# Kernel optimization log

Measured on AMD Instinct MI355X. Metric: run time of the kernel, lower is better.

Reference implementation:

```python
import jax, jax.numpy as jnp
import numpy as np

K_NEIGHBORS = 8   # num_neighbors init arg
BETA = 0.5        # smooth-L1 beta
EPS = 1e-8        # torch cosine_similarity eps


def setup_inputs() -> dict:
    key = jax.random.key(0)
    k1, k2, k3 = jax.random.split(key, 3)
    B, N, D, C = 16, 1024, 768, 2
    return {
        "student_emb": jax.random.normal(k1, (B, N, D), dtype=jnp.float32),
        "teacher_emb": jax.random.normal(k2, (B, N, D), dtype=jnp.float32),
        "centers": jax.random.normal(k3, (B, N, C), dtype=jnp.float32),
    }


def _cosine(anchor, nb):
    # anchor [B,N,1,D], nb [B,N,K,D] -> [B,N,K]
    dot = jnp.sum(anchor * nb, axis=-1)
    na = jnp.maximum(jnp.linalg.norm(anchor, axis=-1), EPS)
    nb_n = jnp.maximum(jnp.linalg.norm(nb, axis=-1), EPS)
    return dot / (na * nb_n)


def reference(student_emb, teacher_emb, centers):
    B, N, _ = centers.shape
    k = min(K_NEIGHBORS + 1, N)
    # brute-force pairwise squared distances [B,N,N] (knn_points)
    sq = jnp.sum(centers * centers, axis=-1)
    d2 = sq[:, :, None] + sq[:, None, :] - 2.0 * jnp.einsum("bnc,bmc->bnm", centers, centers)
    _, idx = jax.lax.top_k(-d2, k)   # ascending distance; idx [B,N,k]
    idx = idx[:, :, 1:]               # drop self (distance 0 is first)
    # knn_gather: neighbors [B,N,K,D]
    gather = jax.vmap(lambda e, i: e[i])
    student_nb = gather(student_emb, idx)
    teacher_nb = gather(teacher_emb, idx)
    student_rel = _cosine(student_emb[:, :, None, :], student_nb)  # [B,N,K]
    teacher_rel = jax.lax.stop_gradient(_cosine(teacher_emb[:, :, None, :], teacher_nb))
    diff = jnp.abs(student_rel - teacher_rel)
    sl1 = jnp.where(diff < BETA, 0.5 * diff * diff / BETA, diff - 0.5 * BETA)
    per_patch = sl1.mean(axis=-1)  # [B,N]
    return per_patch.mean()        # reduction='mean'
```

## Files before the change

kernel.cpp:

```cpp
#include <hip/hip_runtime.h>
#include <hip/hip_fp16.h>
#include <math.h>

#define BB 16
#define NN 1024
#define DD 768
#define KK 8
#define BETA_F 0.5f
#define EPS_F 1e-8f

#define TPK_BLOCKS ((BB * NN) / 8)
#define NORM_BLOCKS ((BB * NN) / 4)

typedef _Float16 h2_t __attribute__((ext_vector_type(2)));

#if defined(__has_builtin)
#if __has_builtin(__builtin_amdgcn_fdot2)
#define HAVE_FDOT2 1
#endif
#endif

__device__ __forceinline__ float dot4acc(uint2 a, uint2 b, float acc) {
#ifdef HAVE_FDOT2
    acc = __builtin_amdgcn_fdot2(__builtin_bit_cast(h2_t, a.x),
                                 __builtin_bit_cast(h2_t, b.x), acc, false);
    acc = __builtin_amdgcn_fdot2(__builtin_bit_cast(h2_t, a.y),
                                 __builtin_bit_cast(h2_t, b.y), acc, false);
#else
    float2 fa = __half22float2(__builtin_bit_cast(__half2, a.x));
    float2 fb = __half22float2(__builtin_bit_cast(__half2, b.x));
    acc = fmaf(fa.x, fb.x, acc); acc = fmaf(fa.y, fb.y, acc);
    fa = __half22float2(__builtin_bit_cast(__half2, a.y));
    fb = __half22float2(__builtin_bit_cast(__half2, b.y));
    acc = fmaf(fa.x, fb.x, acc); acc = fmaf(fa.y, fb.y, acc);
#endif
    return acc;
}

__device__ __forceinline__ unsigned wave_min_u32_to_all(unsigned x) {
    int v = (int)x;
#define STEP(CTRL, RM) {                                                    \
        int y_ = __builtin_amdgcn_update_dpp(v, v, CTRL, RM, 0xf, false);   \
        v = (int)((unsigned)v < (unsigned)y_ ? (unsigned)v : (unsigned)y_); \
    }
    STEP(0x111, 0xf)
    STEP(0x112, 0xf)
    STEP(0x114, 0xf)
    STEP(0x118, 0xf)
    STEP(0x142, 0xa)
    STEP(0x143, 0xc)
#undef STEP
    return (unsigned)__builtin_amdgcn_readlane(v, 63);
}

__device__ __forceinline__ unsigned topk_u(float anx, float any_, float sqn, float4 c) {
    float dot = anx * c.x + any_ * c.y;
    float d2  = (sqn + c.z) - 2.0f * dot;
    unsigned int u = __float_as_uint(d2);
    u ^= (unsigned int)((int)u >> 31) | 0x80000000u;
    return u;
}

struct KeysU { unsigned k[16]; };

#define PIN_KEYSU(K)                                                        \
    asm("" : "+v"(K.k[0]),  "+v"(K.k[1]),  "+v"(K.k[2]),  "+v"(K.k[3]),    \
             "+v"(K.k[4]),  "+v"(K.k[5]),  "+v"(K.k[6]),  "+v"(K.k[7]),    \
             "+v"(K.k[8]),  "+v"(K.k[9]),  "+v"(K.k[10]), "+v"(K.k[11]),   \
             "+v"(K.k[12]), "+v"(K.k[13]), "+v"(K.k[14]), "+v"(K.k[15]))

__device__ __forceinline__ void initkeysu(KeysU& K, float anx, float any_, float sqn,
                                          const float4* c4, int lane) {
#pragma unroll
    for (int i = 0; i < 16; ++i) {
        const int m_ = i * 64 + lane;
        K.k[i] = topk_u(anx, any_, sqn, c4[m_]);
    }
}

__device__ __forceinline__ unsigned umin2(unsigned a, unsigned b) { return a < b ? a : b; }

__device__ __forceinline__ unsigned mintreeu(const KeysU& K) {
    return umin2(umin2(umin2(umin2(K.k[0], K.k[1]),  umin2(K.k[2], K.k[3])),
                       umin2(umin2(K.k[4], K.k[5]),  umin2(K.k[6], K.k[7]))),
                 umin2(umin2(umin2(K.k[8], K.k[9]),  umin2(K.k[10], K.k[11])),
                       umin2(umin2(K.k[12], K.k[13]), umin2(K.k[14], K.k[15]))));
}

__device__ __forceinline__ void topk_wave_body(const float* __restrict__ centers,
                                               int* __restrict__ idx_out,
                                               int tb, int tid, float4* c4) {
    const int b    = tb >> 7;
    const int grp  = tb & 127;
    const int wave = tid >> 6;
    const int lane = tid & 63;

    const float4* cbase = (const float4*)(centers + (size_t)b * NN * 2);
    for (int i = tid; i < NN / 2; i += 256) {
        float4 v = cbase[i];
        c4[2 * i + 0] = make_float4(v.x, v.y, v.x * v.x + v.y * v.y, 0.f);
        c4[2 * i + 1] = make_float4(v.z, v.w, v.z * v.z + v.w * v.w, 0.f);
    }
    __syncthreads();

    const int nA = grp * 8 + wave * 2;
    const int nB = nA + 1;
    const float4 cA = c4[nA];
    const float4 cB = c4[nB];

    KeysU KA, KB;
    initkeysu(KA, cA.x, cA.y, cA.z, c4, lane);
    initkeysu(KB, cB.x, cB.y, cB.z, c4, lane);
    PIN_KEYSU(KA);
    PIN_KEYSU(KB);

    unsigned lmA = mintreeu(KA);
    unsigned lmB = mintreeu(KB);
    int mmA[9], mmB[9];

#pragma unroll
    for (int r = 0; r < 9; ++r) {
        const unsigned gA = wave_min_u32_to_all(lmA);
        const unsigned gB = wave_min_u32_to_all(lmB);

        unsigned mA = 0xffffffffu, mB = 0xffffffffu;
#pragma unroll
        for (int i = 15; i >= 0; --i) {
            unsigned long long bA = __ballot(KA.k[i] == gA);
            unsigned long long bB = __ballot(KB.k[i] == gB);
            mA = bA ? (unsigned)(i * 64) + (unsigned)__builtin_ctzll(bA) : mA;
            mB = bB ? (unsigned)(i * 64) + (unsigned)__builtin_ctzll(bB) : mB;
        }
        mmA[r] = (int)mA;
        mmB[r] = (int)mB;

        const unsigned iwA = mA >> 6, lwA = mA & 63;
        const unsigned iwB = mB >> 6, lwB = mB & 63;
        const bool winA = ((unsigned)lane == lwA);
        const bool winB = ((unsigned)lane == lwB);
#pragma unroll
        for (int i = 0; i < 16; ++i) {
            KA.k[i] = ((unsigned)i == iwA && winA) ? 0xffffffffu : KA.k[i];
            KB.k[i] = ((unsigned)i == iwB && winB) ? 0xffffffffu : KB.k[i];
        }
        PIN_KEYSU(KA);
        PIN_KEYSU(KB);
        lmA = mintreeu(KA);
        lmB = mintreeu(KB);
    }

    if (lane == 0) {
        int* outp = idx_out + ((size_t)b * NN + nA) * KK;
        ((int4*)outp)[0] = make_int4(mmA[1], mmA[2], mmA[3], mmA[4]);
        ((int4*)outp)[1] = make_int4(mmA[5], mmA[6], mmA[7], mmA[8]);
        ((int4*)outp)[2] = make_int4(mmB[1], mmB[2], mmB[3], mmB[4]);
        ((int4*)outp)[3] = make_int4(mmB[5], mmB[6], mmB[7], mmB[8]);
    }
}

__device__ __forceinline__ void normh_body(const float* __restrict__ s,
                                           const float* __restrict__ t,
                                           __half* __restrict__ ns,
                                           __half* __restrict__ nt,
                                           int nb, int tid) {
    const int row  = nb * 4 + (tid >> 6);
    const int lane = tid & 63;
    const float4* srow = (const float4*)(s + (size_t)row * DD);
    const float4* trow = (const float4*)(t + (size_t)row * DD);
    float4 vs[3], vt[3];
    float ss = 0.f, tt = 0.f;
#pragma unroll
    for (int i = 0; i < 3; ++i) {
        vs[i] = srow[lane + 64 * i];
        vt[i] = trow[lane + 64 * i];
        ss = fmaf(vs[i].x, vs[i].x, fmaf(vs[i].y, vs[i].y,
             fmaf(vs[i].z, vs[i].z, fmaf(vs[i].w, vs[i].w, ss))));
        tt = fmaf(vt[i].x, vt[i].x, fmaf(vt[i].y, vt[i].y,
             fmaf(vt[i].z, vt[i].z, fmaf(vt[i].w, vt[i].w, tt))));
    }
#pragma unroll
    for (int m = 1; m < 64; m <<= 1) {
        ss += __shfl_xor(ss, m);
        tt += __shfl_xor(tt, m);
    }
    const float is_ = 1.0f / fmaxf(sqrtf(ss), EPS_F);
    const float it_ = 1.0f / fmaxf(sqrtf(tt), EPS_F);

    uint2* nsrow = (uint2*)(ns + (size_t)row * DD);
    uint2* ntrow = (uint2*)(nt + (size_t)row * DD);
#pragma unroll
    for (int i = 0; i < 3; ++i) {
        __half2 a0 = __floats2half2_rn(vs[i].x * is_, vs[i].y * is_);
        __half2 a1 = __floats2half2_rn(vs[i].z * is_, vs[i].w * is_);
        __half2 b0 = __floats2half2_rn(vt[i].x * it_, vt[i].y * it_);
        __half2 b1 = __floats2half2_rn(vt[i].z * it_, vt[i].w * it_);
        uint2 ua; ua.x = __builtin_bit_cast(unsigned int, a0);
        ua.y = __builtin_bit_cast(unsigned int, a1);
        uint2 ub; ub.x = __builtin_bit_cast(unsigned int, b0);
        ub.y = __builtin_bit_cast(unsigned int, b1);
        nsrow[lane + 64 * i] = ua;
        ntrow[lane + 64 * i] = ub;
    }
}

__global__ __launch_bounds__(256) void fused_prep(const float* __restrict__ centers,
                                                  const float* __restrict__ s,
                                                  const float* __restrict__ t,
                                                  int* __restrict__ idx_out,
                                                  __half* __restrict__ ns,
                                                  __half* __restrict__ nt) {
    __shared__ float4 c4[NN];
    const int r3 = blockIdx.x % 3;
    const int q3 = blockIdx.x / 3;
    if (r3 == 0)
        topk_wave_body(centers, idx_out, q3, threadIdx.x, c4);
    else
        normh_body(s, t, ns, nt, q3 * 2 + (r3 - 1), threadIdx.x);
}

__global__ __launch_bounds__(256) void topk_kernel(const float* __restrict__ centers,
                                                   int* __restrict__ idx_out) {
    __shared__ float4 c4[NN];
    topk_wave_body(centers, idx_out, blockIdx.x, threadIdx.x, c4);
}

__global__ __launch_bounds__(256) void lossh_kernel(const __half* __restrict__ ns,
                                                    const __half* __restrict__ nt,
                                                    const int* __restrict__ idx,
                                                    float* __restrict__ part) {
    const int bid  = blockIdx.x;
    const int v    = (bid & 7) * 512 + (bid >> 3);
    const int wave = threadIdx.x >> 6;
    const int lane = threadIdx.x & 63;
    const int p    = v * 4 + wave;
    const int base = p & ~(NN - 1);

    int q[8];
    {
        const int4* ip = (const int4*)(idx + (size_t)p * KK);
        int4 a = ip[0], c = ip[1];
        q[0] = base + a.x; q[1] = base + a.y; q[2] = base + a.z; q[3] = base + a.w;
        q[4] = base + c.x; q[5] = base + c.y; q[6] = base + c.z; q[7] = base + c.w;
    }

    const uint2* srow = (const uint2*)(ns + (size_t)p * DD);
    const uint2* trow = (const uint2*)(nt + (size_t)p * DD);
    uint2 sa[3], ta[3];
#pragma unroll
    for (int c = 0; c < 3; ++c) {
        sa[c] = srow[lane + 64 * c];
        ta[c] = trow[lane + 64 * c];
    }

    uint2 sv[8][3], tv[8][3];
#pragma unroll
    for (int j = 0; j < 8; ++j) {
        const uint2* snb = (const uint2*)(ns + (size_t)q[j] * DD);
        const uint2* tnb = (const uint2*)(nt + (size_t)q[j] * DD);
#pragma unroll
        for (int c = 0; c < 3; ++c) {
            sv[j][c] = snb[lane + 64 * c];
            tv[j][c] = tnb[lane + 64 * c];
        }
    }

    float ds[8], dt[8];
#pragma unroll
    for (int j = 0; j < 8; ++j) {
        float a = 0.f, b = 0.f;
#pragma unroll
        for (int c = 0; c < 3; ++c) {
            a = dot4acc(sa[c], sv[j][c], a);
            b = dot4acc(ta[c], tv[j][c], b);
        }
        ds[j] = a;
        dt[j] = b;
    }
#pragma unroll
    for (int m = 1; m < 64; m <<= 1) {
#pragma unroll
        for (int j = 0; j < 8; ++j) {
            ds[j] += __shfl_xor(ds[j], m);
            dt[j] += __shfl_xor(dt[j], m);
        }
    }
    float sum = 0.f;
#pragma unroll
    for (int j = 0; j < 8; ++j) {
        const float diff = fabsf(ds[j] - dt[j]);
        sum += diff < BETA_F ? (0.5f * diff * diff / BETA_F) : (diff - 0.5f * BETA_F);
    }

    __shared__ float wpart[4];
    if (lane == 0) wpart[wave] = sum;
    __syncthreads();
    if (threadIdx.x == 0)
        part[v] = (wpart[0] + wpart[1]) + (wpart[2] + wpart[3]);
}

__global__ __launch_bounds__(256) void norm_kernel(const float* __restrict__ s,
                                                   const float* __restrict__ t,
                                                   float* __restrict__ inv_s,
                                                   float* __restrict__ inv_t) {
    const int row  = blockIdx.x * 4 + (threadIdx.x >> 6);
    const int lane = threadIdx.x & 63;
    const float4* srow = (const float4*)(s + (size_t)row * DD);
    const float4* trow = (const float4*)(t + (size_t)row * DD);
    float ss = 0.f, tt = 0.f;
#pragma unroll
    for (int i = 0; i < 3; ++i) {
        float4 v = srow[lane + 64 * i];
        ss = fmaf(v.x, v.x, fmaf(v.y, v.y, fmaf(v.z, v.z, fmaf(v.w, v.w, ss))));
        float4 w = trow[lane + 64 * i];
        tt = fmaf(w.x, w.x, fmaf(w.y, w.y, fmaf(w.z, w.z, fmaf(w.w, w.w, tt))));
    }
#pragma unroll
    for (int m = 1; m < 64; m <<= 1) {
        ss += __shfl_xor(ss, m);
        tt += __shfl_xor(tt, m);
    }
    if (lane == 0) {
        inv_s[row] = 1.0f / fmaxf(sqrtf(ss), EPS_F);
        inv_t[row] = 1.0f / fmaxf(sqrtf(tt), EPS_F);
    }
}

__global__ __launch_bounds__(256) void lossf_kernel(const float* __restrict__ s,
                                                    const float* __restrict__ t,
                                                    const int* __restrict__ idx,
                                                    const float* __restrict__ inv_s,
                                                    const float* __restrict__ inv_t,
                                                    float* __restrict__ part) {
    const int wave = threadIdx.x >> 6;
    const int lane = threadIdx.x & 63;
    const int p    = blockIdx.x * 4 + wave;
    const int base = p & ~(NN - 1);
    int q[8];
    {
        const int4* ip = (const int4*)(idx + (size_t)p * KK);
        int4 a = ip[0], c = ip[1];
        q[0] = base + a.x; q[1] = base + a.y; q[2] = base + a.z; q[3] = base + a.w;
        q[4] = base + c.x; q[5] = base + c.y; q[6] = base + c.z; q[7] = base + c.w;
    }
    float isq[8], itq[8];
#pragma unroll
    for (int j = 0; j < 8; ++j) { isq[j] = inv_s[q[j]]; itq[j] = inv_t[q[j]]; }
    const float isn = inv_s[p];
    const float itn = inv_t[p];
    const float4* srow = (const float4*)(s + (size_t)p * DD);
    const float4* trow = (const float4*)(t + (size_t)p * DD);
    float4 as0 = srow[lane], as1 = srow[lane + 64], as2 = srow[lane + 128];
    float4 at0 = trow[lane], at1 = trow[lane + 64], at2 = trow[lane + 128];
    float ds[8], dt[8];
#pragma unroll
    for (int j = 0; j < 8; ++j) {
        const float4* snb = (const float4*)(s + (size_t)q[j] * DD);
        const float4* tnb = (const float4*)(t + (size_t)q[j] * DD);
        float4 v0 = snb[lane], v1 = snb[lane + 64], v2 = snb[lane + 128];
        float4 w0 = tnb[lane], w1 = tnb[lane + 64], w2 = tnb[lane + 128];
        float a = 0.f, b = 0.f;
        a = fmaf(as0.x, v0.x, a); a = fmaf(as0.y, v0.y, a);
        a = fmaf(as0.z, v0.z, a); a = fmaf(as0.w, v0.w, a);
        a = fmaf(as1.x, v1.x, a); a = fmaf(as1.y, v1.y, a);
        a = fmaf(as1.z, v1.z, a); a = fmaf(as1.w, v1.w, a);
        a = fmaf(as2.x, v2.x, a); a = fmaf(as2.y, v2.y, a);
        a = fmaf(as2.z, v2.z, a); a = fmaf(as2.w, v2.w, a);
        b = fmaf(at0.x, w0.x, b); b = fmaf(at0.y, w0.y, b);
        b = fmaf(at0.z, w0.z, b); b = fmaf(at0.w, w0.w, b);
        b = fmaf(at1.x, w1.x, b); b = fmaf(at1.y, w1.y, b);
        b = fmaf(at1.z, w1.z, b); b = fmaf(at1.w, w1.w, b);
        b = fmaf(at2.x, w2.x, b); b = fmaf(at2.y, w2.y, b);
        b = fmaf(at2.z, w2.z, b); b = fmaf(at2.w, w2.w, b);
        ds[j] = a; dt[j] = b;
    }
#pragma unroll
    for (int m = 1; m < 64; m <<= 1) {
#pragma unroll
        for (int j = 0; j < 8; ++j) {
            ds[j] += __shfl_xor(ds[j], m);
            dt[j] += __shfl_xor(dt[j], m);
        }
    }
    float sum = 0.f;
#pragma unroll
    for (int j = 0; j < 8; ++j) {
        const float cs   = ds[j] * isn * isq[j];
        const float ct   = dt[j] * itn * itq[j];
        const float diff = fabsf(cs - ct);
        sum += diff < BETA_F ? (0.5f * diff * diff / BETA_F) : (diff - 0.5f * BETA_F);
    }
    __shared__ float wpart[4];
    if (lane == 0) wpart[wave] = sum;
    __syncthreads();
    if (threadIdx.x == 0)
        part[blockIdx.x] = (wpart[0] + wpart[1]) + (wpart[2] + wpart[3]);
}

__global__ __launch_bounds__(256) void finalize_kernel(const float* __restrict__ part,
                                                       float* __restrict__ out) {
    __shared__ float red[256];
    float acc = 0.f;
    for (int i = threadIdx.x; i < (BB * NN) / 4; i += 256) acc += part[i];
    red[threadIdx.x] = acc;
    __syncthreads();
    for (int off = 128; off > 0; off >>= 1) {
        if (threadIdx.x < off) red[threadIdx.x] += red[threadIdx.x + off];
        __syncthreads();
    }
    if (threadIdx.x == 0) out[0] = red[0] * (1.0f / (float)(BB * NN * KK));
}

extern "C" void kernel_launch(void* const* d_in, const int* in_sizes, int n_in,
                              void* d_out, int out_size, void* d_ws, size_t ws_size,
                              hipStream_t stream) {
    const float* student = (const float*)d_in[0];
    const float* teacher = (const float*)d_in[1];
    const float* centers = (const float*)d_in[2];
    float* out = (float*)d_out;

    const size_t idx_bytes  = (size_t)BB * NN * KK * sizeof(int);
    const size_t half_bytes = (size_t)BB * NN * DD * sizeof(__half);
    const size_t part_bytes = 4096 * sizeof(float);
    int* idx_buf = (int*)d_ws;

    if (ws_size >= idx_bytes + 2 * half_bytes + part_bytes) {
        __half* ns  = (__half*)((char*)d_ws + idx_bytes);
        __half* nt  = ns + (size_t)BB * NN * DD;
        float* part = (float*)((char*)d_ws + idx_bytes + 2 * half_bytes);
        fused_prep<<<TPK_BLOCKS + NORM_BLOCKS, 256, 0, stream>>>(centers, student,
                                                                 teacher, idx_buf, ns, nt);
        lossh_kernel<<<NORM_BLOCKS, 256, 0, stream>>>(ns, nt, idx_buf, part);
        finalize_kernel<<<1, 256, 0, stream>>>(part, out);
    } else {
        float* inv_s = (float*)((char*)d_ws + idx_bytes);
        float* inv_t = inv_s + BB * NN;
        float* part  = inv_t + BB * NN;
        topk_kernel<<<TPK_BLOCKS, 256, 0, stream>>>(centers, idx_buf);
        norm_kernel<<<NORM_BLOCKS, 256, 0, stream>>>(student, teacher, inv_s, inv_t);
        lossf_kernel<<<NORM_BLOCKS, 256, 0, stream>>>(student, teacher, idx_buf,
                                                      inv_s, inv_t, part);
        finalize_kernel<<<1, 256, 0, stream>>>(part, out);
    }
}
```

Measured before the change: 81.87 us.

## Split fused prep into separate top-k and normalize kernels, roll selection loop

Replaces the single fused_prep kernel, which interleaved top-k blocks and normalization blocks in one launch, with two separate launches: topk_kernel and normh_kernel. It also removes the inline-asm register pinning of the key arrays, stops unrolling the 9-round selection loop, and writes each neighbor index to global memory as soon as it is found instead of buffering them and storing int4 vectors at the end. This trades the overlap of compute-bound top-k with bandwidth-bound normalization for smaller code and possibly lower register pressure. It adds a kernel launch boundary and uses scalar stores.

```diff
diff --git a/kernel.cpp b/kernel.cpp
--- a/kernel.cpp
+++ b/kernel.cpp
@@ -63,12 +63,6 @@
 
 struct KeysU { unsigned k[16]; };
 
-#define PIN_KEYSU(K)                                                        \
-    asm("" : "+v"(K.k[0]),  "+v"(K.k[1]),  "+v"(K.k[2]),  "+v"(K.k[3]),    \
-             "+v"(K.k[4]),  "+v"(K.k[5]),  "+v"(K.k[6]),  "+v"(K.k[7]),    \
-             "+v"(K.k[8]),  "+v"(K.k[9]),  "+v"(K.k[10]), "+v"(K.k[11]),   \
-             "+v"(K.k[12]), "+v"(K.k[13]), "+v"(K.k[14]), "+v"(K.k[15]))
-
 __device__ __forceinline__ void initkeysu(KeysU& K, float anx, float any_, float sqn,
                                           const float4* c4, int lane) {
 #pragma unroll
@@ -111,14 +105,14 @@
     KeysU KA, KB;
     initkeysu(KA, cA.x, cA.y, cA.z, c4, lane);
     initkeysu(KB, cB.x, cB.y, cB.z, c4, lane);
-    PIN_KEYSU(KA);
-    PIN_KEYSU(KB);
 
     unsigned lmA = mintreeu(KA);
     unsigned lmB = mintreeu(KB);
-    int mmA[9], mmB[9];
-
-#pragma unroll
+
+    int* rowA = idx_out + ((size_t)b * NN + nA) * KK;
+    int* rowB = rowA + KK;
+
+#pragma unroll 1
     for (int r = 0; r < 9; ++r) {
         const unsigned gA = wave_min_u32_to_all(lmA);
         const unsigned gB = wave_min_u32_to_all(lmB);
@@ -131,8 +125,11 @@
             mA = bA ? (unsigned)(i * 64) + (unsigned)__builtin_ctzll(bA) : mA;
             mB = bB ? (unsigned)(i * 64) + (unsigned)__builtin_ctzll(bB) : mB;
         }
-        mmA[r] = (int)mA;
-        mmB[r] = (int)mB;
+
+        if (r > 0 && lane == 0) {
+            rowA[r - 1] = (int)mA;
+            rowB[r - 1] = (int)mB;
+        }
 
         const unsigned iwA = mA >> 6, lwA = mA & 63;
         const unsigned iwB = mB >> 6, lwB = mB & 63;
@@ -143,28 +140,23 @@
             KA.k[i] = ((unsigned)i == iwA && winA) ? 0xffffffffu : KA.k[i];
             KB.k[i] = ((unsigned)i == iwB && winB) ? 0xffffffffu : KB.k[i];
         }
-        PIN_KEYSU(KA);
-        PIN_KEYSU(KB);
         lmA = mintreeu(KA);
         lmB = mintreeu(KB);
     }
-
-    if (lane == 0) {
-        int* outp = idx_out + ((size_t)b * NN + nA) * KK;
-        ((int4*)outp)[0] = make_int4(mmA[1], mmA[2], mmA[3], mmA[4]);
-        ((int4*)outp)[1] = make_int4(mmA[5], mmA[6], mmA[7], mmA[8]);
-        ((int4*)outp)[2] = make_int4(mmB[1], mmB[2], mmB[3], mmB[4]);
-        ((int4*)outp)[3] = make_int4(mmB[5], mmB[6], mmB[7], mmB[8]);
-    }
-}
-
-__device__ __forceinline__ void normh_body(const float* __restrict__ s,
-                                           const float* __restrict__ t,
-                                           __half* __restrict__ ns,
-                                           __half* __restrict__ nt,
-                                           int nb, int tid) {
-    const int row  = nb * 4 + (tid >> 6);
-    const int lane = tid & 63;
+}
+
+__global__ __launch_bounds__(256) void topk_kernel(const float* __restrict__ centers,
+                                                   int* __restrict__ idx_out) {
+    __shared__ float4 c4[NN];
+    topk_wave_body(centers, idx_out, blockIdx.x, threadIdx.x, c4);
+}
+
+__global__ __launch_bounds__(256) void normh_kernel(const float* __restrict__ s,
+                                                    const float* __restrict__ t,
+                                                    __half* __restrict__ ns,
+                                                    __half* __restrict__ nt) {
+    const int row  = blockIdx.x * 4 + (threadIdx.x >> 6);
+    const int lane = threadIdx.x & 63;
     const float4* srow = (const float4*)(s + (size_t)row * DD);
     const float4* trow = (const float4*)(t + (size_t)row * DD);
     float4 vs[3], vt[3];
@@ -201,27 +193,6 @@
         nsrow[lane + 64 * i] = ua;
         ntrow[lane + 64 * i] = ub;
     }
-}
-
-__global__ __launch_bounds__(256) void fused_prep(const float* __restrict__ centers,
-                                                  const float* __restrict__ s,
-                                                  const float* __restrict__ t,
-                                                  int* __restrict__ idx_out,
-                                                  __half* __restrict__ ns,
-                                                  __half* __restrict__ nt) {
-    __shared__ float4 c4[NN];
-    const int r3 = blockIdx.x % 3;
-    const int q3 = blockIdx.x / 3;
-    if (r3 == 0)
-        topk_wave_body(centers, idx_out, q3, threadIdx.x, c4);
-    else
-        normh_body(s, t, ns, nt, q3 * 2 + (r3 - 1), threadIdx.x);
-}
-
-__global__ __launch_bounds__(256) void topk_kernel(const float* __restrict__ centers,
-                                                   int* __restrict__ idx_out) {
-    __shared__ float4 c4[NN];
-    topk_wave_body(centers, idx_out, blockIdx.x, threadIdx.x, c4);
 }
 
 __global__ __launch_bounds__(256) void lossh_kernel(const __half* __restrict__ ns,
@@ -427,8 +398,8 @@
         __half* ns  = (__half*)((char*)d_ws + idx_bytes);
         __half* nt  = ns + (size_t)BB * NN * DD;
         float* part = (float*)((char*)d_ws + idx_bytes + 2 * half_bytes);
-        fused_prep<<<TPK_BLOCKS + NORM_BLOCKS, 256, 0, stream>>>(centers, student,
-                                                                 teacher, idx_buf, ns, nt);
+        topk_kernel<<<TPK_BLOCKS, 256, 0, stream>>>(centers, idx_buf);
+        normh_kernel<<<NORM_BLOCKS, 256, 0, stream>>>(student, teacher, ns, nt);
         lossh_kernel<<<NORM_BLOCKS, 256, 0, stream>>>(ns, nt, idx_buf, part);
         finalize_kernel<<<1, 256, 0, stream>>>(part, out);
     } else {
```

Measured after the change: 98.52 us. 20.3% more time.
